# Kernel tuning notes

Measured on AMD Instinct MI355X. Metric: run time of the kernel, lower is better.

## Reference

```python
import jax, jax.numpy as jnp
import numpy as np

N_NODES = 10000
N_EDGES = 160000
F_DIM = 64
H = 4


def setup_inputs() -> dict:
    key = jax.random.key(0)
    ks = jax.random.split(key, 10)
    s = 1.0 / np.sqrt(F_DIM)  # xavier-ish scale
    return {
        "x": jax.random.normal(ks[0], (N_NODES, F_DIM), jnp.float32),
        "edge_index": jax.random.randint(ks[1], (2, N_EDGES), 0, N_NODES),
        "edge_vec": jax.random.normal(ks[2], (N_EDGES, 3), jnp.float32),
        "edge_len": jax.random.uniform(ks[3], (N_EDGES,), jnp.float32, 0.1, 5.0),
        "w_proj_W": jax.random.normal(ks[4], (H, F_DIM, F_DIM), jnp.float32) * s,
        "radial_W": jax.random.normal(ks[5], (H, F_DIM, F_DIM), jnp.float32) * s,
        "tangential_W": jax.random.normal(ks[6], (H, F_DIM, F_DIM), jnp.float32) * s,
        "radial_score": jax.random.normal(ks[7], (H, F_DIM), jnp.float32) * s,
        "tangential_score": jax.random.normal(ks[8], (H, F_DIM), jnp.float32) * s,
        "radial_distance_log_scale": jnp.zeros((), jnp.float32),
        "radial_temp_bias": jnp.zeros((H,), jnp.float32),
        "radial_temp_weight": jnp.zeros((H,), jnp.float32),
        "w_out_W": jax.random.normal(ks[9], (F_DIM, F_DIM), jnp.float32) * s,
    }


def _segment_softmax(logits, receiver, num_nodes):
    # logits: [E, H]; softmax over all edges sharing the same receiver.
    # Equivalent to the original's degree-bucketed per-group softmax.
    m = jax.ops.segment_max(logits, receiver, num_segments=num_nodes)  # [N, H]
    a = jnp.exp(logits - m[receiver])
    d = jax.ops.segment_sum(a, receiver, num_segments=num_nodes)       # [N, H]
    return a / d[receiver]


def reference(x, edge_index, edge_vec, edge_len, w_proj_W, radial_W, tangential_W,
              radial_score, tangential_score, radial_distance_log_scale,
              radial_temp_bias, radial_temp_weight, w_out_W):
    sender, receiver = edge_index[0], edge_index[1]
    n = x.shape[0]

    # Per-head bias-free linear projections (o3.Linear on scalar irreps).
    energy = jnp.einsum('nf,hfg->hng', x, w_proj_W)       # [H, N, F]
    radial = jnp.einsum('nf,hfg->hng', x, radial_W)       # [H, N, F]
    tang = jnp.einsum('nf,hfg->hng', x, tangential_W)     # [H, N, F]

    e_d = energy[:, sender] - energy[:, receiver]                       # [H, E, F]
    r_d = jnp.transpose(radial[:, sender] - radial[:, receiver], (1, 0, 2))  # [E, H, F]
    t_d = jnp.transpose(tang[:, sender] - tang[:, receiver], (1, 0, 2))      # [E, H, F]

    scale = jax.nn.softplus(radial_distance_log_scale)
    r_log = jnp.einsum('hef,hf->eh', e_d, radial_score) - scale * edge_len[:, None]  # [E, H]
    temp = jax.nn.softplus(radial_temp_bias[None, :] + radial_temp_weight[None, :] * edge_len[:, None])
    r_log = r_log / (temp + 0.0001)
    t_log = jnp.einsum('hef,hf->eh', e_d, tangential_score)                          # [E, H]

    r_alpha = _segment_softmax(r_log, receiver, n)  # [E, H]
    t_alpha = _segment_softmax(t_log, receiver, n)  # [E, H]

    r_msg = jax.ops.segment_sum(r_alpha[:, :, None] * r_d, receiver, num_segments=n)  # [N, H, F]
    t_msg = jax.ops.segment_sum(t_alpha[:, :, None] * t_d, receiver, num_segments=n)  # [N, H, F]

    out = jnp.nan_to_num((r_msg + t_msg).mean(axis=1))  # mean over heads -> [N, F]
    return x + out @ w_out_W
```

## Files before the change

### kernel.cpp

```cpp
#include <hip/hip_runtime.h>
#include <math.h>

#define N_NODES 10000
#define N_EDGES 160000
#define CAP 64

typedef short bf16x8 __attribute__((ext_vector_type(8)));
typedef float f32x4 __attribute__((ext_vector_type(4)));

__device__ __forceinline__ float bf2f(unsigned short u) {
    return __uint_as_float(((unsigned int)u) << 16);
}
__device__ __forceinline__ unsigned short f2bf(float f) {
    unsigned int x = __float_as_uint(f);
    unsigned int r = (x + 0x7fffu + ((x >> 16) & 1u)) >> 16;
    return (unsigned short)r;
}
__device__ __forceinline__ float softplus_f(float x) {
    return fmaxf(x, 0.f) + log1pf(expf(-fabsf(x)));
}

#define NB_PROJ 628
#define NB_SCORE 40
#define NB_BUCKET 625

__global__ void __launch_bounds__(256) k_prep(const float* __restrict__ x,
                                              const float* __restrict__ wrad,
                                              const float* __restrict__ wtan,
                                              const float* __restrict__ wproj,
                                              const float* __restrict__ rsc,
                                              const float* __restrict__ tsc,
                                              const int* __restrict__ ei,
                                              const float* __restrict__ el,
                                              unsigned short* __restrict__ radb,
                                              unsigned short* __restrict__ tanb,
                                              float* __restrict__ rs,
                                              float* __restrict__ ts,
                                              int* __restrict__ cur,
                                              int2* __restrict__ sbuf) {
    __shared__ __align__(16) char smem[2 * 64 * 72 * 2];
    int b = blockIdx.x;
    int t = threadIdx.x;

    if (b < NB_PROJ) {
        unsigned short* wt0 = (unsigned short*)smem;
        unsigned short* wt1 = wt0 + 64 * 72;
        int h = b & 3;
        int nb = (b >> 2) * 64;
        const float* wr = wrad + h * 4096;
        const float* wtp = wtan + h * 4096;
        for (int i = 0; i < 16; ++i) {
            int e = t + 256 * i;
            int f = e >> 6, g = e & 63;
            wt0[g * 72 + f] = f2bf(wr[e]);
            wt1[g * 72 + f] = f2bf(wtp[e]);
        }
        __syncthreads();

        int wid = t >> 6, lane = t & 63;
        int q = lane >> 4, l16 = lane & 15;
        int node = nb + wid * 16 + l16;
        int nrow = min(node, N_NODES - 1);

        bf16x8 bfr[2];
#pragma unroll
        for (int kc = 0; kc < 2; ++kc) {
            const float* xp = x + nrow * 64 + kc * 32 + q * 8;
            float4 v0 = ((const float4*)xp)[0];
            float4 v1 = ((const float4*)xp)[1];
            bf16x8 bv;
            bv[0] = (short)f2bf(v0.x); bv[1] = (short)f2bf(v0.y);
            bv[2] = (short)f2bf(v0.z); bv[3] = (short)f2bf(v0.w);
            bv[4] = (short)f2bf(v1.x); bv[5] = (short)f2bf(v1.y);
            bv[6] = (short)f2bf(v1.z); bv[7] = (short)f2bf(v1.w);
            bfr[kc] = bv;
        }
#pragma unroll
        for (int gt = 0; gt < 4; ++gt) {
            f32x4 accr = {0.f, 0.f, 0.f, 0.f};
            f32x4 acct = {0.f, 0.f, 0.f, 0.f};
            int arow = gt * 16 + l16;
#pragma unroll
            for (int kc = 0; kc < 2; ++kc) {
                bf16x8 ar = *(const bf16x8*)&wt0[arow * 72 + kc * 32 + q * 8];
                bf16x8 at = *(const bf16x8*)&wt1[arow * 72 + kc * 32 + q * 8];
                accr = __builtin_amdgcn_mfma_f32_16x16x32_bf16(ar, bfr[kc], accr, 0, 0, 0);
                acct = __builtin_amdgcn_mfma_f32_16x16x32_bf16(at, bfr[kc], acct, 0, 0, 0);
            }
            if (node < N_NODES) {
                int g = gt * 16 + q * 4;
                ushort4 rv = make_ushort4(f2bf(accr[0]), f2bf(accr[1]),
                                          f2bf(accr[2]), f2bf(accr[3]));
                ushort4 tv = make_ushort4(f2bf(acct[0]), f2bf(acct[1]),
                                          f2bf(acct[2]), f2bf(acct[3]));
                *(ushort4*)(radb + node * 256 + h * 64 + g) = rv;
                *(ushort4*)(tanb + node * 256 + h * 64 + g) = tv;
            }
        }
    } else if (b < NB_PROJ + NB_SCORE) {
        float* vrl = (float*)smem;
        float* vtl = vrl + 256;
        {
            int h = t >> 6, f = t & 63;
            const float* wrow = wproj + h * 4096 + f * 64;
            const float* rsp = rsc + h * 64;
            const float* tsp = tsc + h * 64;
            float ar = 0.f, at = 0.f;
            for (int g = 0; g < 64; ++g) {
                float w = wrow[g];
                ar += w * rsp[g];
                at += w * tsp[g];
            }
            vrl[t] = ar;
            vtl[t] = at;
        }
        __syncthreads();
        int n = (b - NB_PROJ) * 256 + t;
        if (n >= N_NODES) return;
        const float4* xr = (const float4*)(x + n * 64);
        float accr[4] = {0.f, 0.f, 0.f, 0.f};
        float acct[4] = {0.f, 0.f, 0.f, 0.f};
        for (int i = 0; i < 16; ++i) {
            float4 xv = xr[i];
#pragma unroll
            for (int h = 0; h < 4; ++h) {
                float4 a = ((const float4*)vrl)[h * 16 + i];
                accr[h] += xv.x * a.x + xv.y * a.y + xv.z * a.z + xv.w * a.w;
                float4 bb = ((const float4*)vtl)[h * 16 + i];
                acct[h] += xv.x * bb.x + xv.y * bb.y + xv.z * bb.z + xv.w * bb.w;
            }
        }
        ((float4*)rs)[n] = make_float4(accr[0], accr[1], accr[2], accr[3]);
        ((float4*)ts)[n] = make_float4(acct[0], acct[1], acct[2], acct[3]);
    } else {
        int e = (b - NB_PROJ - NB_SCORE) * 256 + t;
        if (e >= N_EDGES) return;
        int s = ei[e];
        int r = ei[N_EDGES + e];
        float len = el[e];
        int pos = atomicAdd(&cur[r], 1);
        if (pos < CAP) sbuf[r * CAP + pos] = make_int2(s, __float_as_int(len));
    }
}

__global__ void __launch_bounds__(256) k_node(const int* __restrict__ cur,
                                              const int2* __restrict__ sbuf,
                                              const float* __restrict__ rs,
                                              const float* __restrict__ ts,
                                              const unsigned short* __restrict__ radb,
                                              const unsigned short* __restrict__ tanb,
                                              const float* __restrict__ rdls,
                                              const float* __restrict__ tb,
                                              const float* __restrict__ tw,
                                              const float* __restrict__ x,
                                              const float* __restrict__ wout,
                                              float* __restrict__ out) {
    __shared__ float wl[4096];
    __shared__ float alds[4][CAP][8];
    __shared__ int   slds[4][CAP];
    __shared__ float prelds[4][64];
    int t = threadIdx.x;
    for (int i = 0; i < 16; ++i) wl[t + 256 * i] = wout[t + 256 * i];

    int wid = t >> 6, lane = t & 63;
    int n = blockIdx.x * 4 + wid;
    int deg = min(cur[n], CAP);

    float4 rsr = ((const float4*)rs)[n];
    float4 tsr = ((const float4*)ts)[n];
    float scale = softplus_f(rdls[0]);
    float tb0 = tb[0], tb1 = tb[1], tb2 = tb[2], tb3 = tb[3];
    float tw0 = tw[0], tw1 = tw[1], tw2 = tw[2], tw3 = tw[3];

    const float NEG = -3.402823466e38f;
    float rl0 = NEG, rl1 = NEG, rl2 = NEG, rl3 = NEG;
    float tl0 = NEG, tl1 = NEG, tl2 = NEG, tl3 = NEG;
    int s_e = 0;
    if (lane < deg) {
        int2 sl = sbuf[n * CAP + lane];
        s_e = sl.x;
        float len = __int_as_float(sl.y);
        float4 rss = ((const float4*)rs)[s_e];
        float4 tss = ((const float4*)ts)[s_e];
        float sl0 = scale * len;
        float i0 = 1.f / (softplus_f(tb0 + tw0 * len) + 1e-4f);
        float i1 = 1.f / (softplus_f(tb1 + tw1 * len) + 1e-4f);
        float i2 = 1.f / (softplus_f(tb2 + tw2 * len) + 1e-4f);
        float i3 = 1.f / (softplus_f(tb3 + tw3 * len) + 1e-4f);
        rl0 = ((rss.x - rsr.x) - sl0) * i0;
        rl1 = ((rss.y - rsr.y) - sl0) * i1;
        rl2 = ((rss.z - rsr.z) - sl0) * i2;
        rl3 = ((rss.w - rsr.w) - sl0) * i3;
        tl0 = tss.x - tsr.x;
        tl1 = tss.y - tsr.y;
        tl2 = tss.z - tsr.z;
        tl3 = tss.w - tsr.w;
    }
    float mr0 = rl0, mr1 = rl1, mr2 = rl2, mr3 = rl3;
    float mt0 = tl0, mt1 = tl1, mt2 = tl2, mt3 = tl3;
#pragma unroll
    for (int d = 32; d >= 1; d >>= 1) {
        mr0 = fmaxf(mr0, __shfl_xor(mr0, d)); mr1 = fmaxf(mr1, __shfl_xor(mr1, d));
        mr2 = fmaxf(mr2, __shfl_xor(mr2, d)); mr3 = fmaxf(mr3, __shfl_xor(mr3, d));
        mt0 = fmaxf(mt0, __shfl_xor(mt0, d)); mt1 = fmaxf(mt1, __shfl_xor(mt1, d));
        mt2 = fmaxf(mt2, __shfl_xor(mt2, d)); mt3 = fmaxf(mt3, __shfl_xor(mt3, d));
    }
    float er0 = 0.f, er1 = 0.f, er2 = 0.f, er3 = 0.f;
    float et0 = 0.f, et1 = 0.f, et2 = 0.f, et3 = 0.f;
    if (lane < deg) {
        er0 = expf(rl0 - mr0); er1 = expf(rl1 - mr1);
        er2 = expf(rl2 - mr2); er3 = expf(rl3 - mr3);
        et0 = expf(tl0 - mt0); et1 = expf(tl1 - mt1);
        et2 = expf(tl2 - mt2); et3 = expf(tl3 - mt3);
    }
    float sr0 = er0, sr1 = er1, sr2 = er2, sr3 = er3;
    float st0 = et0, st1 = et1, st2 = et2, st3 = et3;
#pragma unroll
    for (int d = 32; d >= 1; d >>= 1) {
        sr0 += __shfl_xor(sr0, d); sr1 += __shfl_xor(sr1, d);
        sr2 += __shfl_xor(sr2, d); sr3 += __shfl_xor(sr3, d);
        st0 += __shfl_xor(st0, d); st1 += __shfl_xor(st1, d);
        st2 += __shfl_xor(st2, d); st3 += __shfl_xor(st3, d);
    }
    if (lane < deg) {
        float* ap = &alds[wid][lane][0];
        ((float4*)ap)[0] = make_float4(er0 / sr0, er1 / sr1, er2 / sr2, er3 / sr3);
        ((float4*)ap)[1] = make_float4(et0 / st0, et1 / st1, et2 / st2, et3 / st3);
        slds[wid][lane] = s_e;
    }

    int h = lane >> 4;
    int hb = h * 64 + ((lane & 15) << 2);
    float a0 = 0.f, a1 = 0.f, a2 = 0.f, a3 = 0.f;
    float b0 = 0.f, b1 = 0.f, b2 = 0.f, b3 = 0.f;
    int i = 0;
    for (; i + 2 <= deg; i += 2) {
        int s0 = slds[wid][i], s1 = slds[wid][i + 1];
        float ar0 = alds[wid][i][h],     at0 = alds[wid][i][4 + h];
        float ar1 = alds[wid][i + 1][h], at1 = alds[wid][i + 1][4 + h];
        ushort4 rv0 = *(const ushort4*)(radb + s0 * 256 + hb);
        ushort4 tv0 = *(const ushort4*)(tanb + s0 * 256 + hb);
        ushort4 rv1 = *(const ushort4*)(radb + s1 * 256 + hb);
        ushort4 tv1 = *(const ushort4*)(tanb + s1 * 256 + hb);
        a0 += ar0 * bf2f(rv0.x) + ar1 * bf2f(rv1.x);
        a1 += ar0 * bf2f(rv0.y) + ar1 * bf2f(rv1.y);
        a2 += ar0 * bf2f(rv0.z) + ar1 * bf2f(rv1.z);
        a3 += ar0 * bf2f(rv0.w) + ar1 * bf2f(rv1.w);
        b0 += at0 * bf2f(tv0.x) + at1 * bf2f(tv1.x);
        b1 += at0 * bf2f(tv0.y) + at1 * bf2f(tv1.y);
        b2 += at0 * bf2f(tv0.z) + at1 * bf2f(tv1.z);
        b3 += at0 * bf2f(tv0.w) + at1 * bf2f(tv1.w);
    }
    if (i < deg) {
        int s0 = slds[wid][i];
        float ar0 = alds[wid][i][h], at0 = alds[wid][i][4 + h];
        ushort4 rv0 = *(const ushort4*)(radb + s0 * 256 + hb);
        ushort4 tv0 = *(const ushort4*)(tanb + s0 * 256 + hb);
        a0 += ar0 * bf2f(rv0.x); a1 += ar0 * bf2f(rv0.y);
        a2 += ar0 * bf2f(rv0.z); a3 += ar0 * bf2f(rv0.w);
        b0 += at0 * bf2f(tv0.x); b1 += at0 * bf2f(tv0.y);
        b2 += at0 * bf2f(tv0.z); b3 += at0 * bf2f(tv0.w);
    }
    if (deg > 0) {
        ushort4 rv = *(const ushort4*)(radb + n * 256 + hb);
        ushort4 tv = *(const ushort4*)(tanb + n * 256 + hb);
        a0 -= bf2f(rv.x); a1 -= bf2f(rv.y); a2 -= bf2f(rv.z); a3 -= bf2f(rv.w);
        b0 -= bf2f(tv.x); b1 -= bf2f(tv.y); b2 -= bf2f(tv.z); b3 -= bf2f(tv.w);
    }
    float c0 = a0 + b0, c1 = a1 + b1, c2 = a2 + b2, c3 = a3 + b3;
    c0 += __shfl_xor(c0, 16); c0 += __shfl_xor(c0, 32);
    c1 += __shfl_xor(c1, 16); c1 += __shfl_xor(c1, 32);
    c2 += __shfl_xor(c2, 16); c2 += __shfl_xor(c2, 32);
    c3 += __shfl_xor(c3, 16); c3 += __shfl_xor(c3, 32);
    if (lane < 16) {
        ((float4*)&prelds[wid][0])[lane] =
            make_float4(c0 * 0.25f, c1 * 0.25f, c2 * 0.25f, c3 * 0.25f);
    }
    __syncthreads();

    float acc = 0.f;
    const float* pw = &prelds[wid][0];
#pragma unroll 4
    for (int gc = 0; gc < 16; ++gc) {
        float4 pv = ((const float4*)pw)[gc];
        acc += pv.x * wl[(4 * gc + 0) * 64 + lane];
        acc += pv.y * wl[(4 * gc + 1) * 64 + lane];
        acc += pv.z * wl[(4 * gc + 2) * 64 + lane];
        acc += pv.w * wl[(4 * gc + 3) * 64 + lane];
    }
    out[n * 64 + lane] = x[n * 64 + lane] + acc;
}

extern "C" void kernel_launch(void* const* d_in, const int* in_sizes, int n_in,
                              void* d_out, int out_size, void* d_ws, size_t ws_size,
                              hipStream_t stream) {
    const float* x     = (const float*)d_in[0];
    const int*   ei    = (const int*)d_in[1];
    const float* el    = (const float*)d_in[3];
    const float* wproj = (const float*)d_in[4];
    const float* wrad  = (const float*)d_in[5];
    const float* wtan  = (const float*)d_in[6];
    const float* rsc   = (const float*)d_in[7];
    const float* tsc   = (const float*)d_in[8];
    const float* rdls  = (const float*)d_in[9];
    const float* tb    = (const float*)d_in[10];
    const float* tw    = (const float*)d_in[11];
    const float* wout  = (const float*)d_in[12];
    float* out = (float*)d_out;

    char* w = (char*)d_ws;
    size_t o = 0;
    auto nxt = [&](size_t bytes) -> char* {
        char* p = w + o;
        o += (bytes + 255) & ~(size_t)255;
        return p;
    };
    unsigned short* radb = (unsigned short*)nxt((size_t)N_NODES * 256 * 2);
    unsigned short* tanb = (unsigned short*)nxt((size_t)N_NODES * 256 * 2);
    float* rs = (float*)nxt((size_t)N_NODES * 4 * 4);
    float* ts = (float*)nxt((size_t)N_NODES * 4 * 4);
    int*   cur = (int*)nxt((size_t)N_NODES * 4);
    int2*  sbuf = (int2*)nxt((size_t)N_NODES * CAP * 8);

    hipMemsetAsync(cur, 0, (size_t)N_NODES * 4, stream);

    k_prep<<<NB_PROJ + NB_SCORE + NB_BUCKET, 256, 0, stream>>>(
        x, wrad, wtan, wproj, rsc, tsc, ei, el, radb, tanb, rs, ts, cur, sbuf);
    k_node<<<2500, 256, 0, stream>>>(cur, sbuf, rs, ts, radb, tanb,
                                     rdls, tb, tw, x, wout, out);
}
```

Baseline: 132.9 us.

## Fuse prep and node kernels into one persistent kernel with grid barriers

Replaces the memset plus two kernel launches with a single persistent kernel of 768 blocks that zeroes the degree counters, runs the projection, score and bucketing tasks in a grid-stride loop, and then runs the per-node aggregation after a software grid barrier built on global atomics. The goal is to remove launch overhead and the inter-kernel gap, and to load the output weight matrix into shared memory once per block instead of once per node tile. In exchange, correctness depends on all 768 blocks being co-resident, and the barrier adds spin-wait cost. The persistent blocks may also lose some of the latency hiding that 2500 independent blocks provided.

```diff
diff --git a/kernel.cpp b/kernel.cpp
--- a/kernel.cpp
+++ b/kernel.cpp
@@ -4,6 +4,13 @@
 #define N_NODES 10000
 #define N_EDGES 160000
 #define CAP 64
+#define GRID 768
+
+#define NB_PROJ 628
+#define NB_SCORE 40
+#define NB_BUCKET 625
+#define NTASK1 (NB_PROJ + NB_SCORE + NB_BUCKET)
+#define NB_NODE 2500
 
 typedef short bf16x8 __attribute__((ext_vector_type(8)));
 typedef float f32x4 __attribute__((ext_vector_type(4)));
@@ -20,275 +27,298 @@
     return fmaxf(x, 0.f) + log1pf(expf(-fabsf(x)));
 }
 
-#define NB_PROJ 628
-#define NB_SCORE 40
-#define NB_BUCKET 625
-
-__global__ void __launch_bounds__(256) k_prep(const float* __restrict__ x,
-                                              const float* __restrict__ wrad,
-                                              const float* __restrict__ wtan,
-                                              const float* __restrict__ wproj,
-                                              const float* __restrict__ rsc,
-                                              const float* __restrict__ tsc,
-                                              const int* __restrict__ ei,
-                                              const float* __restrict__ el,
-                                              unsigned short* __restrict__ radb,
-                                              unsigned short* __restrict__ tanb,
-                                              float* __restrict__ rs,
-                                              float* __restrict__ ts,
-                                              int* __restrict__ cur,
-                                              int2* __restrict__ sbuf) {
-    __shared__ __align__(16) char smem[2 * 64 * 72 * 2];
+__device__ unsigned int g_cnt = 0;
+__device__ unsigned int g_sense = 0;
+
+__device__ __forceinline__ void gbar() {
+    __syncthreads();
+    if (threadIdx.x == 0) {
+        unsigned int e = __hip_atomic_load(&g_sense, __ATOMIC_ACQUIRE, __HIP_MEMORY_SCOPE_AGENT);
+        unsigned int old = __hip_atomic_fetch_add(&g_cnt, 1, __ATOMIC_ACQ_REL, __HIP_MEMORY_SCOPE_AGENT);
+        if (old == GRID - 1) {
+            __hip_atomic_store(&g_cnt, 0, __ATOMIC_RELAXED, __HIP_MEMORY_SCOPE_AGENT);
+            __hip_atomic_fetch_add(&g_sense, 1, __ATOMIC_RELEASE, __HIP_MEMORY_SCOPE_AGENT);
+        } else {
+            while (__hip_atomic_load(&g_sense, __ATOMIC_ACQUIRE, __HIP_MEMORY_SCOPE_AGENT) == e)
+                __builtin_amdgcn_s_sleep(1);
+        }
+    }
+    __syncthreads();
+}
+
+__global__ void __launch_bounds__(256, 4) k_fused(const float* __restrict__ x,
+                                                  const int* __restrict__ ei,
+                                                  const float* __restrict__ el,
+                                                  const float* __restrict__ wproj,
+                                                  const float* __restrict__ wrad,
+                                                  const float* __restrict__ wtan,
+                                                  const float* __restrict__ rsc,
+                                                  const float* __restrict__ tsc,
+                                                  const float* __restrict__ rdls,
+                                                  const float* __restrict__ tb,
+                                                  const float* __restrict__ tw,
+                                                  const float* __restrict__ wout,
+                                                  unsigned short* __restrict__ radb,
+                                                  unsigned short* __restrict__ tanb,
+                                                  float* __restrict__ rs,
+                                                  float* __restrict__ ts,
+                                                  int* __restrict__ cur,
+                                                  int2* __restrict__ sbuf,
+                                                  float* __restrict__ out) {
+    __shared__ __align__(16) char smem[26624];
     int b = blockIdx.x;
     int t = threadIdx.x;
-
-    if (b < NB_PROJ) {
-        unsigned short* wt0 = (unsigned short*)smem;
-        unsigned short* wt1 = wt0 + 64 * 72;
-        int h = b & 3;
-        int nb = (b >> 2) * 64;
-        const float* wr = wrad + h * 4096;
-        const float* wtp = wtan + h * 4096;
-        for (int i = 0; i < 16; ++i) {
-            int e = t + 256 * i;
-            int f = e >> 6, g = e & 63;
-            wt0[g * 72 + f] = f2bf(wr[e]);
-            wt1[g * 72 + f] = f2bf(wtp[e]);
-        }
-        __syncthreads();
-
-        int wid = t >> 6, lane = t & 63;
-        int q = lane >> 4, l16 = lane & 15;
-        int node = nb + wid * 16 + l16;
-        int nrow = min(node, N_NODES - 1);
-
-        bf16x8 bfr[2];
-#pragma unroll
-        for (int kc = 0; kc < 2; ++kc) {
-            const float* xp = x + nrow * 64 + kc * 32 + q * 8;
-            float4 v0 = ((const float4*)xp)[0];
-            float4 v1 = ((const float4*)xp)[1];
-            bf16x8 bv;
-            bv[0] = (short)f2bf(v0.x); bv[1] = (short)f2bf(v0.y);
-            bv[2] = (short)f2bf(v0.z); bv[3] = (short)f2bf(v0.w);
-            bv[4] = (short)f2bf(v1.x); bv[5] = (short)f2bf(v1.y);
-            bv[6] = (short)f2bf(v1.z); bv[7] = (short)f2bf(v1.w);
-            bfr[kc] = bv;
-        }
-#pragma unroll
-        for (int gt = 0; gt < 4; ++gt) {
-            f32x4 accr = {0.f, 0.f, 0.f, 0.f};
-            f32x4 acct = {0.f, 0.f, 0.f, 0.f};
-            int arow = gt * 16 + l16;
+    int wid = t >> 6, lane = t & 63;
+
+    {
+        int idx = b * 256 + t;
+        if (idx < N_NODES) cur[idx] = 0;
+    }
+    gbar();
+
+    for (int task = b; task < NTASK1; task += GRID) {
+        if (task < NB_PROJ) {
+            unsigned short* wt0 = (unsigned short*)smem;
+            unsigned short* wt1 = wt0 + 64 * 72;
+            int h = task & 3;
+            int nb = (task >> 2) * 64;
+            const float* wr = wrad + h * 4096;
+            const float* wtp = wtan + h * 4096;
+            for (int i = 0; i < 16; ++i) {
+                int e = t + 256 * i;
+                int f = e >> 6, g = e & 63;
+                wt0[g * 72 + f] = f2bf(wr[e]);
+                wt1[g * 72 + f] = f2bf(wtp[e]);
+            }
+            __syncthreads();
+
+            int q = lane >> 4, l16 = lane & 15;
+            int node = nb + wid * 16 + l16;
+            int nrow = min(node, N_NODES - 1);
+
+            bf16x8 bfr[2];
 #pragma unroll
             for (int kc = 0; kc < 2; ++kc) {
-                bf16x8 ar = *(const bf16x8*)&wt0[arow * 72 + kc * 32 + q * 8];
-                bf16x8 at = *(const bf16x8*)&wt1[arow * 72 + kc * 32 + q * 8];
-                accr = __builtin_amdgcn_mfma_f32_16x16x32_bf16(ar, bfr[kc], accr, 0, 0, 0);
-                acct = __builtin_amdgcn_mfma_f32_16x16x32_bf16(at, bfr[kc], acct, 0, 0, 0);
-            }
-            if (node < N_NODES) {
-                int g = gt * 16 + q * 4;
-                ushort4 rv = make_ushort4(f2bf(accr[0]), f2bf(accr[1]),
-                                          f2bf(accr[2]), f2bf(accr[3]));
-                ushort4 tv = make_ushort4(f2bf(acct[0]), f2bf(acct[1]),
-                                          f2bf(acct[2]), f2bf(acct[3]));
-                *(ushort4*)(radb + node * 256 + h * 64 + g) = rv;
-                *(ushort4*)(tanb + node * 256 + h * 64 + g) = tv;
-            }
-        }
-    } else if (b < NB_PROJ + NB_SCORE) {
-        float* vrl = (float*)smem;
-        float* vtl = vrl + 256;
-        {
-            int h = t >> 6, f = t & 63;
-            const float* wrow = wproj + h * 4096 + f * 64;
-            const float* rsp = rsc + h * 64;
-            const float* tsp = tsc + h * 64;
-            float ar = 0.f, at = 0.f;
-            for (int g = 0; g < 64; ++g) {
-                float w = wrow[g];
-                ar += w * rsp[g];
-                at += w * tsp[g];
-            }
-            vrl[t] = ar;
-            vtl[t] = at;
-        }
-        __syncthreads();
-        int n = (b - NB_PROJ) * 256 + t;
-        if (n >= N_NODES) return;
-        const float4* xr = (const float4*)(x + n * 64);
-        float accr[4] = {0.f, 0.f, 0.f, 0.f};
-        float acct[4] = {0.f, 0.f, 0.f, 0.f};
-        for (int i = 0; i < 16; ++i) {
-            float4 xv = xr[i];
-#pragma unroll
-            for (int h = 0; h < 4; ++h) {
-                float4 a = ((const float4*)vrl)[h * 16 + i];
-                accr[h] += xv.x * a.x + xv.y * a.y + xv.z * a.z + xv.w * a.w;
-                float4 bb = ((const float4*)vtl)[h * 16 + i];
-                acct[h] += xv.x * bb.x + xv.y * bb.y + xv.z * bb.z + xv.w * bb.w;
-            }
-        }
-        ((float4*)rs)[n] = make_float4(accr[0], accr[1], accr[2], accr[3]);
-        ((float4*)ts)[n] = make_float4(acct[0], acct[1], acct[2], acct[3]);
-    } else {
-        int e = (b - NB_PROJ - NB_SCORE) * 256 + t;
-        if (e >= N_EDGES) return;
-        int s = ei[e];
-        int r = ei[N_EDGES + e];
-        float len = el[e];
-        int pos = atomicAdd(&cur[r], 1);
-        if (pos < CAP) sbuf[r * CAP + pos] = make_int2(s, __float_as_int(len));
+                const float* xp = x + nrow * 64 + kc * 32 + q * 8;
+                float4 v0 = ((const float4*)xp)[0];
+                float4 v1 = ((const float4*)xp)[1];
+                bf16x8 bv;
+                bv[0] = (short)f2bf(v0.x); bv[1] = (short)f2bf(v0.y);
+                bv[2] = (short)f2bf(v0.z); bv[3] = (short)f2bf(v0.w);
+                bv[4] = (short)f2bf(v1.x); bv[5] = (short)f2bf(v1.y);
+                bv[6] = (short)f2bf(v1.z); bv[7] = (short)f2bf(v1.w);
+                bfr[kc] = bv;
+            }
+#pragma unroll
+            for (int gt = 0; gt < 4; ++gt) {
+                f32x4 accr = {0.f, 0.f, 0.f, 0.f};
+                f32x4 acct = {0.f, 0.f, 0.f, 0.f};
+                int arow = gt * 16 + l16;
+#pragma unroll
+                for (int kc = 0; kc < 2; ++kc) {
+                    bf16x8 ar = *(const bf16x8*)&wt0[arow * 72 + kc * 32 + q * 8];
+                    bf16x8 at = *(const bf16x8*)&wt1[arow * 72 + kc * 32 + q * 8];
+                    accr = __builtin_amdgcn_mfma_f32_16x16x32_bf16(ar, bfr[kc], accr, 0, 0, 0);
+                    acct = __builtin_amdgcn_mfma_f32_16x16x32_bf16(at, bfr[kc], acct, 0, 0, 0);
+                }
+                if (node < N_NODES) {
+                    int g = gt * 16 + q * 4;
+                    ushort4 rv = make_ushort4(f2bf(accr[0]), f2bf(accr[1]),
+                                              f2bf(accr[2]), f2bf(accr[3]));
+                    ushort4 tv = make_ushort4(f2bf(acct[0]), f2bf(acct[1]),
+                                              f2bf(acct[2]), f2bf(acct[3]));
+                    *(ushort4*)(radb + node * 256 + h * 64 + g) = rv;
+                    *(ushort4*)(tanb + node * 256 + h * 64 + g) = tv;
+                }
+            }
+            __syncthreads();
+        } else if (task < NB_PROJ + NB_SCORE) {
+            float* vrl = (float*)smem;
+            float* vtl = vrl + 256;
+            {
+                int h = t >> 6, f = t & 63;
+                const float* wrow = wproj + h * 4096 + f * 64;
+                const float* rsp = rsc + h * 64;
+                const float* tsp = tsc + h * 64;
+                float ar = 0.f, at = 0.f;
+                for (int g = 0; g < 64; ++g) {
+                    float w = wrow[g];
+                    ar += w * rsp[g];
+                    at += w * tsp[g];
+                }
+                vrl[t] = ar;
+                vtl[t] = at;
+            }
+            __syncthreads();
+            int n = (task - NB_PROJ) * 256 + t;
+            if (n < N_NODES) {
+                const float4* xr = (const float4*)(x + n * 64);
+                float accr[4] = {0.f, 0.f, 0.f, 0.f};
+                float acct[4] = {0.f, 0.f, 0.f, 0.f};
+                for (int i = 0; i < 16; ++i) {
+                    float4 xv = xr[i];
+#pragma unroll
+                    for (int h = 0; h < 4; ++h) {
+                        float4 a = ((const float4*)vrl)[h * 16 + i];
+                        accr[h] += xv.x * a.x + xv.y * a.y + xv.z * a.z + xv.w * a.w;
+                        float4 bb = ((const float4*)vtl)[h * 16 + i];
+                        acct[h] += xv.x * bb.x + xv.y * bb.y + xv.z * bb.z + xv.w * bb.w;
+                    }
+                }
+                ((float4*)rs)[n] = make_float4(accr[0], accr[1], accr[2], accr[3]);
+                ((float4*)ts)[n] = make_float4(acct[0], acct[1], acct[2], acct[3]);
+            }
+            __syncthreads();
+        } else {
+            int e = (task - NB_PROJ - NB_SCORE) * 256 + t;
+            if (e < N_EDGES) {
+                int s = ei[e];
+                int r = ei[N_EDGES + e];
+                float len = el[e];
+                int pos = atomicAdd(&cur[r], 1);
+                if (pos < CAP) sbuf[r * CAP + pos] = make_int2(s, __float_as_int(len));
+            }
+        }
     }
-}
-
-__global__ void __launch_bounds__(256) k_node(const int* __restrict__ cur,
-                                              const int2* __restrict__ sbuf,
-                                              const float* __restrict__ rs,
-                                              const float* __restrict__ ts,
-                                              const unsigned short* __restrict__ radb,
-                                              const unsigned short* __restrict__ tanb,
-                                              const float* __restrict__ rdls,
-                                              const float* __restrict__ tb,
-                                              const float* __restrict__ tw,
-                                              const float* __restrict__ x,
-                                              const float* __restrict__ wout,
-                                              float* __restrict__ out) {
-    __shared__ float wl[4096];
-    __shared__ float alds[4][CAP][8];
-    __shared__ int   slds[4][CAP];
-    __shared__ float prelds[4][64];
-    int t = threadIdx.x;
+    gbar();
+
+    float* wl = (float*)smem;
+    float* aldsb = (float*)(smem + 16384);
+    int*   sldsb = (int*)(smem + 24576);
+    float* preb = (float*)(smem + 25600);
     for (int i = 0; i < 16; ++i) wl[t + 256 * i] = wout[t + 256 * i];
-
-    int wid = t >> 6, lane = t & 63;
-    int n = blockIdx.x * 4 + wid;
-    int deg = min(cur[n], CAP);
-
-    float4 rsr = ((const float4*)rs)[n];
-    float4 tsr = ((const float4*)ts)[n];
+    __syncthreads();
+
     float scale = softplus_f(rdls[0]);
     float tb0 = tb[0], tb1 = tb[1], tb2 = tb[2], tb3 = tb[3];
     float tw0 = tw[0], tw1 = tw[1], tw2 = tw[2], tw3 = tw[3];
-
-    const float NEG = -3.402823466e38f;
-    float rl0 = NEG, rl1 = NEG, rl2 = NEG, rl3 = NEG;
-    float tl0 = NEG, tl1 = NEG, tl2 = NEG, tl3 = NEG;
-    int s_e = 0;
-    if (lane < deg) {
-        int2 sl = sbuf[n * CAP + lane];
-        s_e = sl.x;
-        float len = __int_as_float(sl.y);
-        float4 rss = ((const float4*)rs)[s_e];
-        float4 tss = ((const float4*)ts)[s_e];
-        float sl0 = scale * len;
-        float i0 = 1.f / (softplus_f(tb0 + tw0 * len) + 1e-4f);
-        float i1 = 1.f / (softplus_f(tb1 + tw1 * len) + 1e-4f);
-        float i2 = 1.f / (softplus_f(tb2 + tw2 * len) + 1e-4f);
-        float i3 = 1.f / (softplus_f(tb3 + tw3 * len) + 1e-4f);
-        rl0 = ((rss.x - rsr.x) - sl0) * i0;
-        rl1 = ((rss.y - rsr.y) - sl0) * i1;
-        rl2 = ((rss.z - rsr.z) - sl0) * i2;
-        rl3 = ((rss.w - rsr.w) - sl0) * i3;
-        tl0 = tss.x - tsr.x;
-        tl1 = tss.y - tsr.y;
-        tl2 = tss.z - tsr.z;
-        tl3 = tss.w - tsr.w;
+    float* alds = aldsb + wid * CAP * 8;
+    int*   slds = sldsb + wid * CAP;
+    float* prelds = preb + wid * 64;
+
+    for (int nt = b; nt < NB_NODE; nt += GRID) {
+        int n = nt * 4 + wid;
+        int deg = min(cur[n], CAP);
+
+        float4 rsr = ((const float4*)rs)[n];
+        float4 tsr = ((const float4*)ts)[n];
+
+        const float NEG = -3.402823466e38f;
+        float rl0 = NEG, rl1 = NEG, rl2 = NEG, rl3 = NEG;
+        float tl0 = NEG, tl1 = NEG, tl2 = NEG, tl3 = NEG;
+        int s_e = 0;
+        if (lane < deg) {
+            int2 sl = sbuf[n * CAP + lane];
+            s_e = sl.x;
+            float len = __int_as_float(sl.y);
+            float4 rss = ((const float4*)rs)[s_e];
+            float4 tss = ((const float4*)ts)[s_e];
+            float sl0 = scale * len;
+            float i0 = 1.f / (softplus_f(tb0 + tw0 * len) + 1e-4f);
+            float i1 = 1.f / (softplus_f(tb1 + tw1 * len) + 1e-4f);
+            float i2 = 1.f / (softplus_f(tb2 + tw2 * len) + 1e-4f);
+            float i3 = 1.f / (softplus_f(tb3 + tw3 * len) + 1e-4f);
+            rl0 = ((rss.x - rsr.x) - sl0) * i0;
+            rl1 = ((rss.y - rsr.y) - sl0) * i1;
+            rl2 = ((rss.z - rsr.z) - sl0) * i2;
+            rl3 = ((rss.w - rsr.w) - sl0) * i3;
+            tl0 = tss.x - tsr.x;
+            tl1 = tss.y - tsr.y;
+            tl2 = tss.z - tsr.z;
+            tl3 = tss.w - tsr.w;
+        }
+        float mr0 = rl0, mr1 = rl1, mr2 = rl2, mr3 = rl3;
+        float mt0 = tl0, mt1 = tl1, mt2 = tl2, mt3 = tl3;
+#pragma unroll
+        for (int d = 32; d >= 1; d >>= 1) {
+            mr0 = fmaxf(mr0, __shfl_xor(mr0, d)); mr1 = fmaxf(mr1, __shfl_xor(mr1, d));
+            mr2 = fmaxf(mr2, __shfl_xor(mr2, d)); mr3 = fmaxf(mr3, __shfl_xor(mr3, d));
+            mt0 = fmaxf(mt0, __shfl_xor(mt0, d)); mt1 = fmaxf(mt1, __shfl_xor(mt1, d));
+            mt2 = fmaxf(mt2, __shfl_xor(mt2, d)); mt3 = fmaxf(mt3, __shfl_xor(mt3, d));
+        }
+        float er0 = 0.f, er1 = 0.f, er2 = 0.f, er3 = 0.f;
+        float et0 = 0.f, et1 = 0.f, et2 = 0.f, et3 = 0.f;
+        if (lane < deg) {
+            er0 = expf(rl0 - mr0); er1 = expf(rl1 - mr1);
+            er2 = expf(rl2 - mr2); er3 = expf(rl3 - mr3);
+            et0 = expf(tl0 - mt0); et1 = expf(tl1 - mt1);
+            et2 = expf(tl2 - mt2); et3 = expf(tl3 - mt3);
+        }
+        float sr0 = er0, sr1 = er1, sr2 = er2, sr3 = er3;
+        float st0 = et0, st1 = et1, st2 = et2, st3 = et3;
+#pragma unroll
+        for (int d = 32; d >= 1; d >>= 1) {
+            sr0 += __shfl_xor(sr0, d); sr1 += __shfl_xor(sr1, d);
+            sr2 += __shfl_xor(sr2, d); sr3 += __shfl_xor(sr3, d);
+            st0 += __shfl_xor(st0, d); st1 += __shfl_xor(st1, d);
+            st2 += __shfl_xor(st2, d); st3 += __shfl_xor(st3, d);
+        }
+        if (lane < deg) {
+            float* ap = alds + lane * 8;
+            ((float4*)ap)[0] = make_float4(er0 / sr0, er1 / sr1, er2 / sr2, er3 / sr3);
+            ((float4*)ap)[1] = make_float4(et0 / st0, et1 / st1, et2 / st2, et3 / st3);
+            slds[lane] = s_e;
+        }
+
+        int h = lane >> 4;
+        int hb = h * 64 + ((lane & 15) << 2);
+        float a0 = 0.f, a1 = 0.f, a2 = 0.f, a3 = 0.f;
+        float b0 = 0.f, b1 = 0.f, b2 = 0.f, b3 = 0.f;
+        int i = 0;
+        for (; i + 2 <= deg; i += 2) {
+            int s0 = slds[i], s1 = slds[i + 1];
+            float ar0 = alds[i * 8 + h],       at0 = alds[i * 8 + 4 + h];
+            float ar1 = alds[(i + 1) * 8 + h], at1 = alds[(i + 1) * 8 + 4 + h];
+            ushort4 rv0 = *(const ushort4*)(radb + s0 * 256 + hb);
+            ushort4 tv0 = *(const ushort4*)(tanb + s0 * 256 + hb);
+            ushort4 rv1 = *(const ushort4*)(radb + s1 * 256 + hb);
+            ushort4 tv1 = *(const ushort4*)(tanb + s1 * 256 + hb);
+            a0 += ar0 * bf2f(rv0.x) + ar1 * bf2f(rv1.x);
+            a1 += ar0 * bf2f(rv0.y) + ar1 * bf2f(rv1.y);
+            a2 += ar0 * bf2f(rv0.z) + ar1 * bf2f(rv1.z);
+            a3 += ar0 * bf2f(rv0.w) + ar1 * bf2f(rv1.w);
+            b0 += at0 * bf2f(tv0.x) + at1 * bf2f(tv1.x);
+            b1 += at0 * bf2f(tv0.y) + at1 * bf2f(tv1.y);
+            b2 += at0 * bf2f(tv0.z) + at1 * bf2f(tv1.z);
+            b3 += at0 * bf2f(tv0.w) + at1 * bf2f(tv1.w);
+        }
+        if (i < deg) {
+            int s0 = slds[i];
+            float ar0 = alds[i * 8 + h], at0 = alds[i * 8 + 4 + h];
+            ushort4 rv0 = *(const ushort4*)(radb + s0 * 256 + hb);
+            ushort4 tv0 = *(const ushort4*)(tanb + s0 * 256 + hb);
+            a0 += ar0 * bf2f(rv0.x); a1 += ar0 * bf2f(rv0.y);
+            a2 += ar0 * bf2f(rv0.z); a3 += ar0 * bf2f(rv0.w);
+            b0 += at0 * bf2f(tv0.x); b1 += at0 * bf2f(tv0.y);
+            b2 += at0 * bf2f(tv0.z); b3 += at0 * bf2f(tv0.w);
+        }
+        if (deg > 0) {
+            ushort4 rv = *(const ushort4*)(radb + n * 256 + hb);
+            ushort4 tv = *(const ushort4*)(tanb + n * 256 + hb);
+            a0 -= bf2f(rv.x); a1 -= bf2f(rv.y); a2 -= bf2f(rv.z); a3 -= bf2f(rv.w);
+            b0 -= bf2f(tv.x); b1 -= bf2f(tv.y); b2 -= bf2f(tv.z); b3 -= bf2f(tv.w);
+        }
+        float c0 = a0 + b0, c1 = a1 + b1, c2 = a2 + b2, c3 = a3 + b3;
+        c0 += __shfl_xor(c0, 16); c0 += __shfl_xor(c0, 32);
+        c1 += __shfl_xor(c1, 16); c1 += __shfl_xor(c1, 32);
+        c2 += __shfl_xor(c2, 16); c2 += __shfl_xor(c2, 32);
+        c3 += __shfl_xor(c3, 16); c3 += __shfl_xor(c3, 32);
+        if (lane < 16) {
+            ((float4*)prelds)[lane] =
+                make_float4(c0 * 0.25f, c1 * 0.25f, c2 * 0.25f, c3 * 0.25f);
+        }
+
+        float acc = 0.f;
+#pragma unroll 4
+        for (int gc = 0; gc < 16; ++gc) {
+            float4 pv = ((const float4*)prelds)[gc];
+            acc += pv.x * wl[(4 * gc + 0) * 64 + lane];
+            acc += pv.y * wl[(4 * gc + 1) * 64 + lane];
+            acc += pv.z * wl[(4 * gc + 2) * 64 + lane];
+            acc += pv.w * wl[(4 * gc + 3) * 64 + lane];
+        }
+        out[n * 64 + lane] = x[n * 64 + lane] + acc;
     }
-    float mr0 = rl0, mr1 = rl1, mr2 = rl2, mr3 = rl3;
-    float mt0 = tl0, mt1 = tl1, mt2 = tl2, mt3 = tl3;
-#pragma unroll
-    for (int d = 32; d >= 1; d >>= 1) {
-        mr0 = fmaxf(mr0, __shfl_xor(mr0, d)); mr1 = fmaxf(mr1, __shfl_xor(mr1, d));
-        mr2 = fmaxf(mr2, __shfl_xor(mr2, d)); mr3 = fmaxf(mr3, __shfl_xor(mr3, d));
-        mt0 = fmaxf(mt0, __shfl_xor(mt0, d)); mt1 = fmaxf(mt1, __shfl_xor(mt1, d));
-        mt2 = fmaxf(mt2, __shfl_xor(mt2, d)); mt3 = fmaxf(mt3, __shfl_xor(mt3, d));
-    }
-    float er0 = 0.f, er1 = 0.f, er2 = 0.f, er3 = 0.f;
-    float et0 = 0.f, et1 = 0.f, et2 = 0.f, et3 = 0.f;
-    if (lane < deg) {
-        er0 = expf(rl0 - mr0); er1 = expf(rl1 - mr1);
-        er2 = expf(rl2 - mr2); er3 = expf(rl3 - mr3);
-        et0 = expf(tl0 - mt0); et1 = expf(tl1 - mt1);
-        et2 = expf(tl2 - mt2); et3 = expf(tl3 - mt3);
-    }
-    float sr0 = er0, sr1 = er1, sr2 = er2, sr3 = er3;
-    float st0 = et0, st1 = et1, st2 = et2, st3 = et3;
-#pragma unroll
-    for (int d = 32; d >= 1; d >>= 1) {
-        sr0 += __shfl_xor(sr0, d); sr1 += __shfl_xor(sr1, d);
-        sr2 += __shfl_xor(sr2, d); sr3 += __shfl_xor(sr3, d);
-        st0 += __shfl_xor(st0, d); st1 += __shfl_xor(st1, d);
-        st2 += __shfl_xor(st2, d); st3 += __shfl_xor(st3, d);
-    }
-    if (lane < deg) {
-        float* ap = &alds[wid][lane][0];
-        ((float4*)ap)[0] = make_float4(er0 / sr0, er1 / sr1, er2 / sr2, er3 / sr3);
-        ((float4*)ap)[1] = make_float4(et0 / st0, et1 / st1, et2 / st2, et3 / st3);
-        slds[wid][lane] = s_e;
-    }
-
-    int h = lane >> 4;
-    int hb = h * 64 + ((lane & 15) << 2);
-    float a0 = 0.f, a1 = 0.f, a2 = 0.f, a3 = 0.f;
-    float b0 = 0.f, b1 = 0.f, b2 = 0.f, b3 = 0.f;
-    int i = 0;
-    for (; i + 2 <= deg; i += 2) {
-        int s0 = slds[wid][i], s1 = slds[wid][i + 1];
-        float ar0 = alds[wid][i][h],     at0 = alds[wid][i][4 + h];
-        float ar1 = alds[wid][i + 1][h], at1 = alds[wid][i + 1][4 + h];
-        ushort4 rv0 = *(const ushort4*)(radb + s0 * 256 + hb);
-        ushort4 tv0 = *(const ushort4*)(tanb + s0 * 256 + hb);
-        ushort4 rv1 = *(const ushort4*)(radb + s1 * 256 + hb);
-        ushort4 tv1 = *(const ushort4*)(tanb + s1 * 256 + hb);
-        a0 += ar0 * bf2f(rv0.x) + ar1 * bf2f(rv1.x);
-        a1 += ar0 * bf2f(rv0.y) + ar1 * bf2f(rv1.y);
-        a2 += ar0 * bf2f(rv0.z) + ar1 * bf2f(rv1.z);
-        a3 += ar0 * bf2f(rv0.w) + ar1 * bf2f(rv1.w);
-        b0 += at0 * bf2f(tv0.x) + at1 * bf2f(tv1.x);
-        b1 += at0 * bf2f(tv0.y) + at1 * bf2f(tv1.y);
-        b2 += at0 * bf2f(tv0.z) + at1 * bf2f(tv1.z);
-        b3 += at0 * bf2f(tv0.w) + at1 * bf2f(tv1.w);
-    }
-    if (i < deg) {
-        int s0 = slds[wid][i];
-        float ar0 = alds[wid][i][h], at0 = alds[wid][i][4 + h];
-        ushort4 rv0 = *(const ushort4*)(radb + s0 * 256 + hb);
-        ushort4 tv0 = *(const ushort4*)(tanb + s0 * 256 + hb);
-        a0 += ar0 * bf2f(rv0.x); a1 += ar0 * bf2f(rv0.y);
-        a2 += ar0 * bf2f(rv0.z); a3 += ar0 * bf2f(rv0.w);
-        b0 += at0 * bf2f(tv0.x); b1 += at0 * bf2f(tv0.y);
-        b2 += at0 * bf2f(tv0.z); b3 += at0 * bf2f(tv0.w);
-    }
-    if (deg > 0) {
-        ushort4 rv = *(const ushort4*)(radb + n * 256 + hb);
-        ushort4 tv = *(const ushort4*)(tanb + n * 256 + hb);
-        a0 -= bf2f(rv.x); a1 -= bf2f(rv.y); a2 -= bf2f(rv.z); a3 -= bf2f(rv.w);
-        b0 -= bf2f(tv.x); b1 -= bf2f(tv.y); b2 -= bf2f(tv.z); b3 -= bf2f(tv.w);
-    }
-    float c0 = a0 + b0, c1 = a1 + b1, c2 = a2 + b2, c3 = a3 + b3;
-    c0 += __shfl_xor(c0, 16); c0 += __shfl_xor(c0, 32);
-    c1 += __shfl_xor(c1, 16); c1 += __shfl_xor(c1, 32);
-    c2 += __shfl_xor(c2, 16); c2 += __shfl_xor(c2, 32);
-    c3 += __shfl_xor(c3, 16); c3 += __shfl_xor(c3, 32);
-    if (lane < 16) {
-        ((float4*)&prelds[wid][0])[lane] =
-            make_float4(c0 * 0.25f, c1 * 0.25f, c2 * 0.25f, c3 * 0.25f);
-    }
-    __syncthreads();
-
-    float acc = 0.f;
-    const float* pw = &prelds[wid][0];
-#pragma unroll 4
-    for (int gc = 0; gc < 16; ++gc) {
-        float4 pv = ((const float4*)pw)[gc];
-        acc += pv.x * wl[(4 * gc + 0) * 64 + lane];
-        acc += pv.y * wl[(4 * gc + 1) * 64 + lane];
-        acc += pv.z * wl[(4 * gc + 2) * 64 + lane];
-        acc += pv.w * wl[(4 * gc + 3) * 64 + lane];
-    }
-    out[n * 64 + lane] = x[n * 64 + lane] + acc;
 }
 
 extern "C" void kernel_launch(void* const* d_in, const int* in_sizes, int n_in,
@@ -322,10 +352,7 @@
     int*   cur = (int*)nxt((size_t)N_NODES * 4);
     int2*  sbuf = (int2*)nxt((size_t)N_NODES * CAP * 8);
 
-    hipMemsetAsync(cur, 0, (size_t)N_NODES * 4, stream);
-
-    k_prep<<<NB_PROJ + NB_SCORE + NB_BUCKET, 256, 0, stream>>>(
-        x, wrad, wtan, wproj, rsc, tsc, ei, el, radb, tanb, rs, ts, cur, sbuf);
-    k_node<<<2500, 256, 0, stream>>>(cur, sbuf, rs, ts, radb, tanb,
-                                     rdls, tb, tw, x, wout, out);
-}
+    k_fused<<<GRID, 256, 0, stream>>>(x, ei, el, wproj, wrad, wtan, rsc, tsc,
+                                      rdls, tb, tw, wout,
+                                      radb, tanb, rs, ts, cur, sbuf, out);
+}
```

Result: slower. 332.9 us (+150.5%).
